# Kernel optimization log

Hardware: AMD Instinct MI355X
Metric: run time of the kernel (lower is better)

Reference implementation:

```python
import jax, jax.numpy as jnp
import numpy as np

NUM_HEADS = 32
EPS = 1e-5
NEG_INF = -1e9


def _ln(x, g, b):
    m = x.mean(-1, keepdims=True)
    v = ((x - m) ** 2).mean(-1, keepdims=True)
    return (x - m) / jnp.sqrt(v + EPS) * g + b


def setup_inputs() -> dict:
    key = jax.random.key(0)
    ks = jax.random.split(key, 20)
    N, B, D, E, F, L = 512, 2, 768, 256, 3072, 4
    inp = {
        'x': jax.random.normal(ks[0], (N, B, D), jnp.float32),
        'pos': jax.random.normal(ks[1], (B, N, 3), jnp.float32) * 5.0,
        'padding_mask': jnp.broadcast_to(jnp.arange(N)[None, :] >= N - 32, (B, N)),
        'outcell_index': jax.random.randint(ks[2], (B, E), 0, N),
        'expand_pos': jax.random.normal(ks[3], (B, E, 3), jnp.float32) * 5.0,
        'expand_mask': jnp.broadcast_to(jnp.arange(E)[None, :] >= E - 16, (B, E)),
        'vec_project_w': jax.random.normal(ks[4], (D, 3 * D), jnp.float32) * 0.02,
        'ln_x_g': jnp.ones((L, D), jnp.float32),
        'ln_x_b': jnp.zeros((L, D), jnp.float32),
        'ln_vec_g': jnp.ones((L, D), jnp.float32),
        'ln_vec_b': jnp.zeros((L, D), jnp.float32),
        'adaln_x_w': jax.random.normal(ks[5], (L, D, D), jnp.float32) * 0.02,
        'adaln_vecmlp_w': jax.random.normal(ks[6], (L, D, 2 * D), jnp.float32) * 0.02,
        'out_proj_w': jax.random.normal(ks[7], (L, D, D), jnp.float32) * 0.02,
        'vecmlp_norm_g': jnp.ones((L, D), jnp.float32),
        'vecmlp_norm_b': jnp.zeros((L, D), jnp.float32),
        'mlp_w1': jax.random.normal(ks[8], (L, D, F), jnp.float32) * 0.02,
        'mlp_w2': jax.random.normal(ks[9], (L, F, D), jnp.float32) * 0.02,
    }
    return inp


def reference(x, pos, padding_mask, outcell_index, expand_pos, expand_mask,
              vec_project_w, ln_x_g, ln_x_b, ln_vec_g, ln_vec_b,
              adaln_x_w, adaln_vecmlp_w, out_proj_w,
              vecmlp_norm_g, vecmlp_norm_b, mlp_w1, mlp_w2):
    x = jnp.swapaxes(x, 0, 1)  # [B,N,D]
    B, N, D = x.shape
    H = NUM_HEADS
    hd = D // H
    L = ln_x_g.shape[0]

    # --- PBC-expanded pairwise distance bias ---
    epf = jnp.concatenate([pos, expand_pos], axis=1)  # [B,S,3]
    S = epf.shape[1]
    delta = pos[:, :, None, :] - epf[:, None, :, :]   # [B,N,S,3]
    sq = (delta * delta).sum(-1)
    dist = jnp.where(sq > 0, jnp.sqrt(jnp.where(sq > 0, sq, 1.0)), 0.0)
    kpm_full = jnp.concatenate([padding_mask, expand_mask], axis=-1)  # [B,S]
    dist = jnp.where(padding_mask[:, :, None], 1e6, dist)
    dist = jnp.where(kpm_full[:, None, :], 1e6, dist)
    dist = 1.0 / (dist + 1.0)
    # additive attn mask (bias + key-padding -inf), broadcast over heads
    attn_mask = jnp.where(kpm_full[:, None, None, :], NEG_INF, dist[:, None, :, :])  # [B,1,N,S]

    vec = (jax.nn.silu(x) @ vec_project_w).reshape(B, N, 3, D)
    barange = jnp.arange(B)[:, None]
    scale = 1.0 / jnp.sqrt(jnp.float32(3 * hd))

    for l in range(L):
        rx, rv = x, vec
        xl = _ln(x, ln_x_g[l], ln_x_b[l])
        vl = _ln(vec, ln_vec_g[l], ln_vec_b[l])
        scale_x = jax.nn.silu(xl) @ adaln_x_w[l]        # [B,N,D]
        vmod = vl * scale_x[:, :, None, :]              # [B,N,3,D]
        # PBC gather-expanded K/V
        kv_exp = vmod[barange, outcell_index]           # [B,E,3,D]
        kv = jnp.concatenate([vmod, kv_exp], axis=1)    # [B,S,3,D]
        q = vmod.reshape(B, N, 3, H, hd).transpose(0, 3, 1, 2, 4).reshape(B, H, N, 3 * hd)
        k = kv.reshape(B, S, 3, H, hd).transpose(0, 3, 1, 2, 4).reshape(B, H, S, 3 * hd)
        v = k  # q=k=v in this block (same modulated vec)
        k = kv.reshape(B, S, 3, H, hd).transpose(0, 3, 1, 2, 4).reshape(B, H, S, 3 * hd)
        logits = jnp.einsum('bhnd,bhsd->bhns', q, k) * scale + attn_mask
        p = jax.nn.softmax(logits, axis=-1)
        o = jnp.einsum('bhns,bhsd->bhnd', p, v)          # [B,H,N,3hd]
        o = o.transpose(0, 2, 1, 3).reshape(B, N, H, 3, hd).transpose(0, 1, 3, 2, 4).reshape(B, N, 3, D)
        o = o @ out_proj_w[l]
        x = xl + rx
        vec = o + rv
        rx, rv = x, vec
        vm = _ln(vec, vecmlp_norm_g[l], vecmlp_norm_b[l])
        vm = jax.nn.silu(vm @ mlp_w1[l]) @ mlp_w2[l]     # [B,N,3,D]
        ss = jax.nn.silu(vm) @ adaln_vecmlp_w[l]         # [B,N,3,2D]
        sc, sh = jnp.split(ss, 2, axis=-1)
        x = x * sc.sum(-2) + sh.sum(-2) + rx
        vec = vm + rv
    return x, vec
```

## Files before the change

kernel.cpp:

```cpp
#include <hip/hip_runtime.h>

typedef __bf16 bf16_t;
typedef __bf16 bf8   __attribute__((ext_vector_type(8)));
typedef __bf16 bf4   __attribute__((ext_vector_type(4)));
typedef float  f32x4 __attribute__((ext_vector_type(4)));

__device__ __forceinline__ f32x4 mfma16(bf8 a, bf8 b, f32x4 c){
  return __builtin_amdgcn_mfma_f32_16x16x32_bf16(a, b, c, 0, 0, 0);
}
__device__ __forceinline__ float siluf_(float x){ return x / (1.f + __expf(-x)); }

__device__ __forceinline__ void async16(bf16_t* lds, const bf16_t* g){
  __builtin_amdgcn_global_load_lds(
      (const __attribute__((address_space(1))) unsigned int*)g,
      (__attribute__((address_space(3))) unsigned int*)lds, 16, 0, 0);
}

#define SCALE_QK 0.1178511302f

#define WT_VP   0ull
#define WT_AX   3538944ull
#define WT_AV   8257536ull
#define WT_OP   17694720ull
#define WT_M1   22413312ull
#define WT_M2   41287680ull
#define MASKB   60162048ull
#define SILUX   63307776ull
#define SILUXL  64880640ull
#define VLB     66453504ull
#define QKHB    79036416ull
#define KVTB    88473600ull
#define OBFB    97910784ull
#define VMLNB   102629376ull
#define H1B     107347968ull
#define SVM2B   126222336ull

struct TD { const float* s; bf16_t* d; int R, C, start, perz; };
struct TPack { TD t[6]; };

#define NTRB 3672

__global__ void prologue(TPack P,
                         const float* __restrict__ pos, const float* __restrict__ epos,
                         bf16_t* __restrict__ wm,
                         const float* __restrict__ xin, float* __restrict__ x,
                         bf16_t* __restrict__ sx,
                         const float* __restrict__ lxg, const float* __restrict__ lxb,
                         bf16_t* __restrict__ siluxl)
{
  __shared__ bf16_t tile[128*72];
  const int bid = blockIdx.x;
  const int t = threadIdx.x;
  if (bid >= NTRB + 3072){
    const int w2 = t >> 6, l = t & 63;
    const int r = (bid - NTRB - 3072)*4 + w2;
    const int b = r >> 9, n = r & 511;
    const float* p = xin + ((size_t)n*2 + b)*768;
    f32x4 v[3]; float s = 0.f;
    #pragma unroll
    for (int ps = 0; ps < 3; ++ps){
      v[ps] = *(const f32x4*)(p + ps*256 + l*4);
      bf4 sb;
      #pragma unroll
      for (int e = 0; e < 4; ++e){ s += v[ps][e]; sb[e] = (bf16_t)siluf_(v[ps][e]); }
      *(bf4*)(sx + (size_t)r*768 + ps*256 + l*4) = sb;
    }
    #pragma unroll
    for (int m = 1; m < 64; m <<= 1) s += __shfl_xor(s, m);
    float mean = s * (1.f/768.f);
    float q = 0.f;
    #pragma unroll
    for (int ps = 0; ps < 3; ++ps)
      #pragma unroll
      for (int e = 0; e < 4; ++e){ float d = v[ps][e] - mean; q += d*d; }
    #pragma unroll
    for (int m = 1; m < 64; m <<= 1) q += __shfl_xor(q, m);
    float rstd = rsqrtf(q * (1.f/768.f) + 1e-5f);
    #pragma unroll
    for (int ps = 0; ps < 3; ++ps){
      int col = ps*256 + l*4;
      f32x4 gg = *(const f32x4*)(lxg + col);
      f32x4 bv = *(const f32x4*)(lxb + col);
      f32x4 xo; bf4 ob;
      #pragma unroll
      for (int e = 0; e < 4; ++e){
        float xl = (v[ps][e] - mean) * rstd * gg[e] + bv[e];
        xo[e] = xl + v[ps][e];
        ob[e] = (bf16_t)siluf_(xl);
      }
      *(f32x4*)(x + (size_t)r*768 + col) = xo;
      *(bf4*)(siluxl + (size_t)r*768 + col) = ob;
    }
    return;
  }
  if (bid >= NTRB){
    int i = (bid - NTRB) * 256 + t;
    int s = i % 768, tt = i / 768;
    int n = tt % 512, b = tt / 512;
    bool kpm = (s < 512) ? (s >= 480) : (s >= 752);
    float o;
    if (kpm) o = 0.f;
    else {
      float d;
      if (n >= 480) d = 1e6f;
      else {
        const float* p = pos + (size_t)(b*512 + n)*3;
        const float* e = (s < 512) ? pos + (size_t)(b*512 + s)*3
                                   : epos + (size_t)(b*256 + (s-512))*3;
        float dx = p[0]-e[0], dy = p[1]-e[1], dz = p[2]-e[2];
        float sq = dx*dx + dy*dy + dz*dz;
        d = sq > 0.f ? sqrtf(sq) : 0.f;
      }
      o = __expf(1.f / (d + 1.f));
    }
    wm[i] = (bf16_t)o;
    return;
  }
  int k = 0;
  #pragma unroll
  for (int i = 1; i < 6; ++i) k = (bid >= P.t[i].start) ? i : k;
  const TD td = P.t[k];
  const int loc = bid - td.start;
  const int z = loc / td.perz, tl = loc - z*td.perz;
  const int nct = td.C >> 7;
  const int cx = tl % nct, ry = tl / nct;
  const size_t base = (size_t)z * td.R * td.C;
  const int r0 = ry*64, c0 = cx*128;
  #pragma unroll
  for (int half = 0; half < 2; ++half){
    int bb = half*256 + t;
    int rb = bb >> 5, cb = bb & 31;
    f32x4 v[4];
    #pragma unroll
    for (int i = 0; i < 4; ++i)
      v[i] = *(const f32x4*)(td.s + base + (size_t)(r0 + rb*4 + i)*td.C + c0 + cb*4);
    const int sw = (cb & 7) << 1;
    const int rp = 4*(rb ^ sw);
    #pragma unroll
    for (int e = 0; e < 4; ++e){
      bf4 pk;
      #pragma unroll
      for (int i = 0; i < 4; ++i) pk[i] = (bf16_t)v[i][e];
      *(bf4*)&tile[(cb*4 + e)*72 + rp] = pk;
    }
  }
  __syncthreads();
  #pragma unroll
  for (int jj = 0; jj < 4; ++jj){
    int sid = jj*256 + t;
    int c = sid >> 3, q = sid & 7;
    int qp = q ^ ((c >> 2) & 7);
    bf8 o = *(const bf8*)&tile[c*72 + qp*8];
    *(bf8*)(td.d + base + (size_t)(c0 + c)*td.R + r0 + q*8) = o;
  }
}

__global__ __launch_bounds__(256,2) void ln_kernel(
    const float* __restrict__ in, const float* __restrict__ g, const float* __restrict__ bb,
    bf16_t* __restrict__ bfout)
{
  const int w = threadIdx.x >> 6, l = threadIdx.x & 63;
  const size_t r = (size_t)blockIdx.x * 4 + w;
  const float* p = in + r * 768;
  f32x4 v[3]; float s = 0.f;
  #pragma unroll
  for (int ps = 0; ps < 3; ++ps){
    v[ps] = *(const f32x4*)(p + ps*256 + l*4);
    #pragma unroll
    for (int e = 0; e < 4; ++e) s += v[ps][e];
  }
  #pragma unroll
  for (int m = 1; m < 64; m <<= 1) s += __shfl_xor(s, m);
  float mean = s * (1.f/768.f);
  float q = 0.f;
  #pragma unroll
  for (int ps = 0; ps < 3; ++ps)
    #pragma unroll
    for (int e = 0; e < 4; ++e){ float d = v[ps][e] - mean; q += d*d; }
  #pragma unroll
  for (int m = 1; m < 64; m <<= 1) q += __shfl_xor(q, m);
  float rstd = rsqrtf(q * (1.f/768.f) + 1e-5f);
  #pragma unroll
  for (int ps = 0; ps < 3; ++ps){
    int col = ps*256 + l*4;
    f32x4 gg = *(const f32x4*)(g + col);
    f32x4 bv = *(const f32x4*)(bb + col);
    bf4 ob;
    #pragma unroll
    for (int e = 0; e < 4; ++e)
      ob[e] = (bf16_t)((v[ps][e] - mean) * rstd * gg[e] + bv[e]);
    *(bf4*)(bfout + r*768 + col) = ob;
  }
}

__global__ __launch_bounds__(256,2) void pack2_kernel(
    const bf16_t* __restrict__ vl, const bf16_t* __restrict__ pq,
    const int* __restrict__ idx, bf16_t* __restrict__ qkh, bf16_t* __restrict__ kvt)
{
  __shared__ bf16_t tile[64*104];
  const int sb = blockIdx.x, bh = blockIdx.y;
  const int b = bh >> 5, h = bh & 31;
  const int tid = threadIdx.x;
  const bf8 z8 = {};
  #pragma unroll
  for (int it = 0; it < 3; ++it){
    int u = it*256 + tid;
    int s_l = u / 12, ch = u % 12;
    int s = sb*64 + s_l;
    bf8 o = z8;
    if (ch < 9){
      int n = (s < 512) ? s : idx[b*256 + (s - 512)];
      int c = ch / 3, jj0 = (ch % 3) * 8;
      int d0 = h*24 + jj0;
      size_t soff = (size_t)(b*512 + n)*768 + d0;
      bf8 a = *(const bf8*)(vl + ((size_t)(b*512 + n)*3 + c)*768 + d0);
      bf8 q0 = *(const bf8*)(pq + soff);
      bf8 q1 = *(const bf8*)(pq + soff + 786432);
      bf8 q2 = *(const bf8*)(pq + soff + 1572864);
      bf8 q3 = *(const bf8*)(pq + soff + 2359296);
      #pragma unroll
      for (int e = 0; e < 8; ++e){
        float sc = (float)q0[e] + (float)q1[e] + (float)q2[e] + (float)q3[e];
        o[e] = (bf16_t)((float)a[e] * sc);
      }
    }
    *(bf8*)(qkh + ((size_t)bh*768 + s)*96 + ch*8) = o;
    *(bf8*)&tile[s_l*104 + ch*8] = o;
  }
  __syncthreads();
  #pragma unroll
  for (int it = 0; it < 3; ++it){
    int u = it*256 + tid;
    int d_r = u / 8, s8 = u % 8;
    bf8 o;
    #pragma unroll
    for (int e = 0; e < 8; ++e) o[e] = tile[(s8*8 + e)*104 + d_r];
    *(bf8*)(kvt + ((size_t)bh*96 + d_r)*768 + sb*64 + s8*8) = o;
  }
}

__global__ __launch_bounds__(256,2) void attn_kernel(
    const bf16_t* __restrict__ qkh, const bf16_t* __restrict__ kvt,
    const bf16_t* __restrict__ wm, bf16_t* __restrict__ obf)
{
  __shared__ bf16_t Ks[64*128];
  __shared__ bf16_t Vs[96*72];
  __shared__ bf16_t Ps[64*72];
  __shared__ bf16_t Ws[64*72];
  const int g = blockIdx.x;
  const int qt = g >> 6, bh = g & 63;
  const int b = bh >> 5, h = bh & 31;
  const int tid = threadIdx.x, w = tid >> 6, l = tid & 63;
  const int lg = l >> 4, lr = l & 15;
  const int qn0 = qt*64 + w*16 + lg*4;

  bf8 aq[3];
  {
    const bf16_t* qb = qkh + ((size_t)bh*768 + qt*64 + w*16 + lr)*96;
    #pragma unroll
    for (int ks = 0; ks < 3; ++ks) aq[ks] = *(const bf8*)(qb + ks*32 + lg*8);
  }

  int klds[3], vlds[3]; size_t kg[3], vg[3];
  #pragma unroll
  for (int it = 0; it < 3; ++it){
    int f = it*256 + tid;
    int r_ = f / 12, c_ = f % 12;
    klds[it] = r_*256 + ((c_*16) ^ ((r_ & 7) << 4));
    kg[it] = ((size_t)bh*768 + r_)*96 + c_*8;
    int vd = f >> 3, vc = (f & 7)*8;
    vlds[it] = vd*72 + vc;
    vg[it] = ((size_t)bh*96 + vd)*768 + vc;
  }
  const bf16_t* wrow = wm + (size_t)b*512*768;
  const int wr_ = tid >> 2, wcq = (tid & 3) * 16;
  const size_t wg0 = (size_t)(qt*64 + wr_)*768 + wcq;
  const int wlds = wr_*72 + wcq;

  f32x4 zf = {0.f,0.f,0.f,0.f};
  f32x4 accO[6];
  #pragma unroll
  for (int i = 0; i < 6; ++i) accO[i] = zf;
  float s_r[4] = {0.f, 0.f, 0.f, 0.f};

  bf8 kr[3], vr[3], wg[2];
  #pragma unroll
  for (int it = 0; it < 3; ++it){
    kr[it] = *(const bf8*)(qkh + kg[it]);
    vr[it] = *(const bf8*)(kvt + vg[it]);
  }
  wg[0] = *(const bf8*)(wrow + wg0);
  wg[1] = *(const bf8*)(wrow + wg0 + 8);
  #pragma unroll
  for (int it = 0; it < 3; ++it){
    *(bf8*)((char*)Ks + klds[it]) = kr[it];
    *(bf8*)&Vs[vlds[it]] = vr[it];
  }
  *(bf8*)&Ws[wlds] = wg[0];
  *(bf8*)&Ws[wlds + 8] = wg[1];
  __syncthreads();

  for (int t = 0; t < 12; ++t){
    const int s0 = t*64;
    if (t < 11){
      #pragma unroll
      for (int it = 0; it < 3; ++it){
        kr[it] = *(const bf8*)(qkh + kg[it] + (size_t)(s0 + 64)*96);
        vr[it] = *(const bf8*)(kvt + vg[it] + (s0 + 64));
      }
      wg[0] = *(const bf8*)(wrow + wg0 + s0 + 64);
      wg[1] = *(const bf8*)(wrow + wg0 + s0 + 72);
    }
    f32x4 sacc[4];
    __builtin_amdgcn_s_setprio(1);
    #pragma unroll
    for (int sf = 0; sf < 4; ++sf){
      sacc[sf] = zf;
      const int row = sf*16 + lr;
      #pragma unroll
      for (int ks = 0; ks < 3; ++ks){
        bf8 bg = *(const bf8*)((const char*)Ks + row*256 + ((ks*64 + lg*16) ^ ((row & 7) << 4)));
        sacc[sf] = mfma16(aq[ks], bg, sacc[sf]);
      }
    }
    __builtin_amdgcn_s_setprio(0);
    #pragma unroll
    for (int sf = 0; sf < 4; ++sf)
      #pragma unroll
      for (int r = 0; r < 4; ++r){
        float p = __expf(sacc[sf][r]*SCALE_QK)
                  * (float)Ws[(w*16 + lg*4 + r)*72 + sf*16 + lr];
        s_r[r] += p;
        Ps[(w*16 + lg*4 + r)*72 + sf*16 + lr] = (bf16_t)p;
      }
    __builtin_amdgcn_s_setprio(1);
    #pragma unroll
    for (int k2 = 0; k2 < 2; ++k2){
      bf8 pa = *(const bf8*)&Ps[(w*16 + lr)*72 + k2*32 + lg*8];
      #pragma unroll
      for (int df = 0; df < 6; ++df)
        accO[df] = mfma16(pa, *(const bf8*)&Vs[(df*16 + lr)*72 + k2*32 + lg*8], accO[df]);
    }
    __builtin_amdgcn_s_setprio(0);
    if (t < 11){
      __syncthreads();
      #pragma unroll
      for (int it = 0; it < 3; ++it){
        *(bf8*)((char*)Ks + klds[it]) = kr[it];
        *(bf8*)&Vs[vlds[it]] = vr[it];
      }
      *(bf8*)&Ws[wlds] = wg[0];
      *(bf8*)&Ws[wlds + 8] = wg[1];
      __syncthreads();
    }
  }
  #pragma unroll
  for (int m = 1; m < 16; m <<= 1)
    #pragma unroll
    for (int r = 0; r < 4; ++r) s_r[r] += __shfl_xor(s_r[r], m);
  float rs[4];
  #pragma unroll
  for (int r = 0; r < 4; ++r) rs[r] = 1.f / s_r[r];
  #pragma unroll
  for (int df = 0; df < 6; ++df){
    int dp = df*16 + lr;
    if (dp < 72){
      int c = dp / 24, jj = dp - c*24;
      #pragma unroll
      for (int r = 0; r < 4; ++r){
        float v = accO[df][r] * rs[r];
        int qn = qn0 + r;
        obf[((size_t)(b*512 + qn)*3 + c)*768 + h*24 + jj] = (bf16_t)v;
      }
    }
  }
}

template<int EPI>
__global__ __launch_bounds__(512,4) void gemm2(
    const bf16_t* __restrict__ A, const bf16_t* __restrict__ Bt,
    float* __restrict__ Cf, bf16_t* __restrict__ Cb,
    int M, int Nn, int K, int Ksub, int ntiles)
{
  __shared__ bf16_t As[128*64];
  __shared__ bf16_t Bs[128*64];
  const int tid = threadIdx.x;
  const int w = tid >> 6, l = tid & 63;
  const int lg = l >> 4, lr = l & 15;
  const int gb = blockIdx.x;
  const int sidx = gb >> 3, xcd = gb & 7;
  const int nt = sidx % ntiles;
  const int mt = xcd + (sidx / ntiles) * 8;
  const int wm = (w >> 2) * 64, wn = (w & 3) * 32;

  const int srow = w*8 + (l >> 3);
  const int scol = (((l & 7) ^ (l >> 3)) << 3);
  const bf16_t* Ab = A  + (size_t)(mt*128) * K;
  const bf16_t* Bb = Bt + (size_t)(nt*128) * K;
  const int kbeg = blockIdx.z * Ksub;

  f32x4 zf = {0.f,0.f,0.f,0.f};
  f32x4 acc[4][2];
  #pragma unroll
  for (int i = 0; i < 4; ++i)
    #pragma unroll
    for (int j = 0; j < 2; ++j) acc[i][j] = zf;

  int offA[4], offB[2];
  #pragma unroll
  for (int i = 0; i < 4; ++i){
    int row = wm + i*16 + lr;
    offA[i] = row*128 + ((lg*16) ^ ((row & 7) << 4));
  }
  #pragma unroll
  for (int j = 0; j < 2; ++j){
    int row = wn + j*16 + lr;
    offB[j] = row*128 + ((lg*16) ^ ((row & 7) << 4));
  }

  for (int k0 = kbeg; k0 < kbeg + Ksub; k0 += 64){
    __syncthreads();
    #pragma unroll
    for (int c = 0; c < 2; ++c){
      async16(&As[c*4096 + w*512], Ab + (size_t)(c*64 + srow)*K + k0 + scol);
      async16(&Bs[c*4096 + w*512], Bb + (size_t)(c*64 + srow)*K + k0 + scol);
    }
    __syncthreads();
    #pragma unroll
    for (int kk = 0; kk < 2; ++kk){
      bf8 af[4], bg[2];
      #pragma unroll
      for (int i = 0; i < 4; ++i)
        af[i] = *(const bf8*)((const char*)As + (offA[i] ^ (kk*64)));
      #pragma unroll
      for (int j = 0; j < 2; ++j)
        bg[j] = *(const bf8*)((const char*)Bs + (offB[j] ^ (kk*64)));
      #pragma unroll
      for (int i = 0; i < 4; ++i)
        #pragma unroll
        for (int j = 0; j < 2; ++j)
          acc[i][j] = mfma16(af[i], bg[j], acc[i][j]);
    }
  }

  const size_t zoff = (EPI == 6) ? (size_t)blockIdx.z * M * Nn : 0;
  #pragma unroll
  for (int i = 0; i < 4; ++i){
    int r0 = mt*128 + wm + i*16 + lg*4;
    #pragma unroll
    for (int j = 0; j < 2; ++j){
      int cc = nt*128 + wn + j*16 + lr;
      #pragma unroll
      for (int r = 0; r < 4; ++r){
        size_t off = (size_t)(r0 + r)*Nn + cc;
        float v = acc[i][j][r];
        if constexpr (EPI == 0)      Cf[off] = v;
        else if constexpr (EPI == 2) Cb[off] = (bf16_t)siluf_(v);
        else                         Cb[zoff + off] = (bf16_t)v;
      }
    }
  }
}

__global__ __launch_bounds__(256,2) void redop_ln(
    const bf16_t* __restrict__ p, float* __restrict__ vec,
    const float* __restrict__ g, const float* __restrict__ bb,
    bf16_t* __restrict__ vmln)
{
  const int w = threadIdx.x >> 6, l = threadIdx.x & 63;
  const size_t r = (size_t)blockIdx.x * 4 + w;
  f32x4 v[3]; float s = 0.f;
  #pragma unroll
  for (int ps = 0; ps < 3; ++ps){
    size_t off = r*768 + ps*256 + l*4;
    bf4 p0 = *(const bf4*)(p + off);
    bf4 p1 = *(const bf4*)(p + off + 2359296);
    bf4 p2 = *(const bf4*)(p + off + 4718592);
    f32x4 vv = *(const f32x4*)(vec + off);
    #pragma unroll
    for (int e = 0; e < 4; ++e){
      float t = vv[e] + (float)p0[e] + (float)p1[e] + (float)p2[e];
      v[ps][e] = t; s += t;
    }
    *(f32x4*)(vec + off) = v[ps];
  }
  #pragma unroll
  for (int m = 1; m < 64; m <<= 1) s += __shfl_xor(s, m);
  float mean = s * (1.f/768.f);
  float q = 0.f;
  #pragma unroll
  for (int ps = 0; ps < 3; ++ps)
    #pragma unroll
    for (int e = 0; e < 4; ++e){ float d = v[ps][e] - mean; q += d*d; }
  #pragma unroll
  for (int m = 1; m < 64; m <<= 1) q += __shfl_xor(q, m);
  float rstd = rsqrtf(q * (1.f/768.f) + 1e-5f);
  #pragma unroll
  for (int ps = 0; ps < 3; ++ps){
    int col = ps*256 + l*4;
    f32x4 gg = *(const f32x4*)(g + col);
    f32x4 bv = *(const f32x4*)(bb + col);
    bf4 ob;
    #pragma unroll
    for (int e = 0; e < 4; ++e)
      ob[e] = (bf16_t)((v[ps][e] - mean) * rstd * gg[e] + bv[e]);
    *(bf4*)(vmln + r*768 + col) = ob;
  }
}

__global__ __launch_bounds__(256,2) void redmlp2_ln(
    const bf16_t* __restrict__ p, float* __restrict__ vec,
    bf16_t* __restrict__ svm2s,
    const float* __restrict__ g, const float* __restrict__ bb,
    bf16_t* __restrict__ vlb, int doln)
{
  const int w = threadIdx.x >> 6, l = threadIdx.x & 63;
  const size_t bn = (size_t)blockIdx.x * 4 + w;
  f32x4 ssum[3];
  #pragma unroll
  for (int ps = 0; ps < 3; ++ps) ssum[ps] = (f32x4){0.f,0.f,0.f,0.f};
  for (int c = 0; c < 3; ++c){
    const size_t r = bn*3 + c;
    f32x4 v[3]; float s = 0.f;
    #pragma unroll
    for (int ps = 0; ps < 3; ++ps){
      size_t off = r*768 + ps*256 + l*4;
      bf4 p0 = *(const bf4*)(p + off);
      bf4 p1 = *(const bf4*)(p + off + 2359296);
      f32x4 vv = *(const f32x4*)(vec + off);
      #pragma unroll
      for (int e = 0; e < 4; ++e){
        float tm = (float)p0[e] + (float)p1[e];
        float t = vv[e] + tm;
        v[ps][e] = t; s += t;
        ssum[ps][e] += siluf_(tm);
      }
      *(f32x4*)(vec + off) = v[ps];
    }
    if (doln){
      #pragma unroll
      for (int m = 1; m < 64; m <<= 1) s += __shfl_xor(s, m);
      float mean = s * (1.f/768.f);
      float q = 0.f;
      #pragma unroll
      for (int ps = 0; ps < 3; ++ps)
        #pragma unroll
        for (int e = 0; e < 4; ++e){ float d = v[ps][e] - mean; q += d*d; }
      #pragma unroll
      for (int m = 1; m < 64; m <<= 1) q += __shfl_xor(q, m);
      float rstd = rsqrtf(q * (1.f/768.f) + 1e-5f);
      #pragma unroll
      for (int ps = 0; ps < 3; ++ps){
        int col = ps*256 + l*4;
        f32x4 gg = *(const f32x4*)(g + col);
        f32x4 bv = *(const f32x4*)(bb + col);
        bf4 ob;
        #pragma unroll
        for (int e = 0; e < 4; ++e)
          ob[e] = (bf16_t)((v[ps][e] - mean) * rstd * gg[e] + bv[e]);
        *(bf4*)(vlb + r*768 + col) = ob;
      }
    }
  }
  #pragma unroll
  for (int ps = 0; ps < 3; ++ps){
    bf4 ob;
    #pragma unroll
    for (int e = 0; e < 4; ++e) ob[e] = (bf16_t)ssum[ps][e];
    *(bf4*)(svm2s + bn*768 + ps*256 + l*4) = ob;
  }
}

__global__ __launch_bounds__(256,2) void comb_ln(
    const bf16_t* __restrict__ p, float* __restrict__ x,
    const float* __restrict__ g, const float* __restrict__ bb,
    bf16_t* __restrict__ siluxl)
{
  const int w = threadIdx.x >> 6, l = threadIdx.x & 63;
  const size_t r = (size_t)blockIdx.x * 4 + w;
  const size_t base = r * 1536;
  f32x4 v[3]; float s = 0.f;
  #pragma unroll
  for (int ps = 0; ps < 3; ++ps){
    int col = ps*256 + l*4;
    bf4 sc0 = *(const bf4*)(p + base + col);
    bf4 sc1 = *(const bf4*)(p + base + col + 1572864);
    bf4 sh0 = *(const bf4*)(p + base + 768 + col);
    bf4 sh1 = *(const bf4*)(p + base + 768 + col + 1572864);
    f32x4 xv = *(const f32x4*)(x + r*768 + col);
    #pragma unroll
    for (int e = 0; e < 4; ++e){
      float t = xv[e]*(1.f + (float)sc0[e] + (float)sc1[e])
              + (float)sh0[e] + (float)sh1[e];
      v[ps][e] = t; s += t;
    }
  }
  #pragma unroll
  for (int m = 1; m < 64; m <<= 1) s += __shfl_xor(s, m);
  float mean = s * (1.f/768.f);
  float q = 0.f;
  #pragma unroll
  for (int ps = 0; ps < 3; ++ps)
    #pragma unroll
    for (int e = 0; e < 4; ++e){ float d = v[ps][e] - mean; q += d*d; }
  #pragma unroll
  for (int m = 1; m < 64; m <<= 1) q += __shfl_xor(q, m);
  float rstd = rsqrtf(q * (1.f/768.f) + 1e-5f);
  #pragma unroll
  for (int ps = 0; ps < 3; ++ps){
    int col = ps*256 + l*4;
    f32x4 gg = *(const f32x4*)(g + col);
    f32x4 bv = *(const f32x4*)(bb + col);
    f32x4 xo; bf4 ob;
    #pragma unroll
    for (int e = 0; e < 4; ++e){
      float xl = (v[ps][e] - mean) * rstd * gg[e] + bv[e];
      xo[e] = xl + v[ps][e];
      ob[e] = (bf16_t)siluf_(xl);
    }
    *(f32x4*)(x + r*768 + col) = xo;
    *(bf4*)(siluxl + r*768 + col) = ob;
  }
}

__global__ void combine_kernel(const bf16_t* __restrict__ p, float* __restrict__ x)
{
  int i = blockIdx.x * 256 + threadIdx.x;
  int row = i / 192, col = (i % 192) * 4;
  size_t base = (size_t)row*1536 + col;
  bf4 sc0 = *(const bf4*)(p + base);
  bf4 sc1 = *(const bf4*)(p + base + 1572864);
  bf4 sh0 = *(const bf4*)(p + base + 768);
  bf4 sh1 = *(const bf4*)(p + base + 768 + 1572864);
  f32x4 xv = *(const f32x4*)(x + (size_t)row*768 + col);
  f32x4 o;
  #pragma unroll
  for (int e = 0; e < 4; ++e)
    o[e] = xv[e]*(1.f + (float)sc0[e] + (float)sc1[e])
         + (float)sh0[e] + (float)sh1[e];
  *(f32x4*)(x + (size_t)row*768 + col) = o;
}

extern "C" void kernel_launch(void* const* d_in, const int* in_sizes, int n_in,
                              void* d_out, int out_size, void* d_ws, size_t ws_size,
                              hipStream_t stream)
{
  const float* x_in = (const float*)d_in[0];
  const float* pos  = (const float*)d_in[1];
  const int*   idx  = (const int*)d_in[3];
  const float* epos = (const float*)d_in[4];
  const float* vp_w = (const float*)d_in[6];
  const float* lxg  = (const float*)d_in[7];
  const float* lxb  = (const float*)d_in[8];
  const float* lvg  = (const float*)d_in[9];
  const float* lvb  = (const float*)d_in[10];
  const float* axw  = (const float*)d_in[11];
  const float* avw  = (const float*)d_in[12];
  const float* opw  = (const float*)d_in[13];
  const float* vng  = (const float*)d_in[14];
  const float* vnb  = (const float*)d_in[15];
  const float* w1   = (const float*)d_in[16];
  const float* w2   = (const float*)d_in[17];

  char* ws = (char*)d_ws;
  bf16_t* wt_vp = (bf16_t*)(ws + WT_VP);
  bf16_t* wt_ax = (bf16_t*)(ws + WT_AX);
  bf16_t* wt_av = (bf16_t*)(ws + WT_AV);
  bf16_t* wt_op = (bf16_t*)(ws + WT_OP);
  bf16_t* wt_m1 = (bf16_t*)(ws + WT_M1);
  bf16_t* wt_m2 = (bf16_t*)(ws + WT_M2);
  bf16_t* wmask = (bf16_t*)(ws + MASKB);
  bf16_t* silux = (bf16_t*)(ws + SILUX);
  bf16_t* siluxl= (bf16_t*)(ws + SILUXL);
  bf16_t* vlb   = (bf16_t*)(ws + VLB);
  bf16_t* qkh   = (bf16_t*)(ws + QKHB);
  bf16_t* kvt   = (bf16_t*)(ws + KVTB);
  bf16_t* partX = (bf16_t*)(ws + H1B);
  bf16_t* partQ = (bf16_t*)(ws + QKHB);
  bf16_t* partV = (bf16_t*)(ws + VLB);
  bf16_t* obf   = (bf16_t*)(ws + OBFB);
  bf16_t* vmln  = (bf16_t*)(ws + VMLNB);
  bf16_t* h1    = (bf16_t*)(ws + H1B);
  bf16_t* svm2s = (bf16_t*)(ws + SVM2B);

  float* x   = (float*)d_out;
  float* vec = x + 786432;

  TPack P;
  P.t[0] = { vp_w, wt_vp, 768, 2304,    0,  216 };
  P.t[1] = { axw,  wt_ax, 768,  768,  216,   72 };
  P.t[2] = { avw,  wt_av, 768, 1536,  504,  144 };
  P.t[3] = { opw,  wt_op, 768,  768, 1080,   72 };
  P.t[4] = { w1,   wt_m1, 768, 3072, 1368,  288 };
  P.t[5] = { w2,   wt_m2, 3072, 768, 2520,  288 };
  prologue<<<NTRB + 3072 + 256, 256, 0, stream>>>(P, pos, epos, wmask, x_in, x, silux,
                                                  lxg, lxb, siluxl);

  gemm2<0><<<dim3(8*18,1,1), 512, 0, stream>>>(silux, wt_vp, vec, nullptr,
                                               1024, 2304, 768, 768, 18);
  ln_kernel<<<768, 256, 0, stream>>>(vec, lvg, lvb, vlb);

  for (int l = 0; l < 4; ++l){
    gemm2<6><<<dim3(8*6,1,4), 512, 0, stream>>>(siluxl, wt_ax + (size_t)l*768*768, nullptr,
                                                partX, 1024, 768, 768, 192, 6);
    pack2_kernel<<<dim3(12, 64), 256, 0, stream>>>(vlb, partX, idx, qkh, kvt);
    attn_kernel<<<512, 256, 0, stream>>>(qkh, kvt, wmask, obf);
    gemm2<6><<<dim3(24*6,1,3), 512, 0, stream>>>(obf, wt_op + (size_t)l*768*768, nullptr,
                                                 partV, 3072, 768, 768, 256, 6);
    redop_ln<<<768, 256, 0, stream>>>(partV, vec, vng + l*768, vnb + l*768, vmln);
    gemm2<2><<<dim3(24*24,1,1), 512, 0, stream>>>(vmln, wt_m1 + (size_t)l*3072*768, nullptr,
                                                  h1, 3072, 3072, 768, 768, 24);
    gemm2<6><<<dim3(24*6,1,2), 512, 0, stream>>>(h1, wt_m2 + (size_t)l*768*3072, nullptr,
                                                 partQ, 3072, 768, 3072, 1536, 6);
    redmlp2_ln<<<256, 256, 0, stream>>>(partQ, vec, svm2s,
                                        lvg + (l+1 < 4 ? (l+1)*768 : 0),
                                        lvb + (l+1 < 4 ? (l+1)*768 : 0),
                                        vlb, (l < 3) ? 1 : 0);
    gemm2<6><<<dim3(8*12,1,2), 512, 0, stream>>>(svm2s, wt_av + (size_t)l*1536*768, nullptr,
                                                 partQ, 1024, 1536, 768, 384, 12);
    if (l < 3)
      comb_ln<<<256, 256, 0, stream>>>(partQ, x, lxg + (l+1)*768, lxb + (l+1)*768, siluxl);
    else
      combine_kernel<<<768, 256, 0, stream>>>(partQ, x);
  }
}
```

Before: 577.0 us.

## Double-buffer GEMM LDS tiles and increase split-K with fused reductions

The GEMM main loop now double-buffers its LDS tiles, issuing async loads for the next K-slice while MFMAs run on the current one. This leaves one barrier per iteration instead of two. The vec-projection GEMM becomes split-K with a new fused reduce+LayerNorm kernel, and the adaLN GEMMs use more K-splits, with consumers summing more partial slices. The cost is twice the LDS per block, which may reduce occupancy, plus more partial-sum traffic.

After: 599.5 us. 1.04x slower.

```diff
diff --git a/kernel.cpp b/kernel.cpp
--- a/kernel.cpp
+++ b/kernel.cpp
@@ -155,19 +155,25 @@
   }
 }
 
-__global__ __launch_bounds__(256,2) void ln_kernel(
-    const float* __restrict__ in, const float* __restrict__ g, const float* __restrict__ bb,
-    bf16_t* __restrict__ bfout)
+__global__ __launch_bounds__(256,2) void redvp_ln(
+    const bf16_t* __restrict__ p, float* __restrict__ vec,
+    const float* __restrict__ g, const float* __restrict__ bb,
+    bf16_t* __restrict__ vlb)
 {
   const int w = threadIdx.x >> 6, l = threadIdx.x & 63;
   const size_t r = (size_t)blockIdx.x * 4 + w;
-  const float* p = in + r * 768;
   f32x4 v[3]; float s = 0.f;
   #pragma unroll
   for (int ps = 0; ps < 3; ++ps){
-    v[ps] = *(const f32x4*)(p + ps*256 + l*4);
-    #pragma unroll
-    for (int e = 0; e < 4; ++e) s += v[ps][e];
+    size_t off = r*768 + ps*256 + l*4;
+    bf4 p0 = *(const bf4*)(p + off);
+    bf4 p1 = *(const bf4*)(p + off + 2359296);
+    #pragma unroll
+    for (int e = 0; e < 4; ++e){
+      float t = (float)p0[e] + (float)p1[e];
+      v[ps][e] = t; s += t;
+    }
+    *(f32x4*)(vec + off) = v[ps];
   }
   #pragma unroll
   for (int m = 1; m < 64; m <<= 1) s += __shfl_xor(s, m);
@@ -189,7 +195,7 @@
     #pragma unroll
     for (int e = 0; e < 4; ++e)
       ob[e] = (bf16_t)((v[ps][e] - mean) * rstd * gg[e] + bv[e]);
-    *(bf4*)(bfout + r*768 + col) = ob;
+    *(bf4*)(vlb + r*768 + col) = ob;
   }
 }
 
@@ -214,15 +220,17 @@
       int d0 = h*24 + jj0;
       size_t soff = (size_t)(b*512 + n)*768 + d0;
       bf8 a = *(const bf8*)(vl + ((size_t)(b*512 + n)*3 + c)*768 + d0);
-      bf8 q0 = *(const bf8*)(pq + soff);
-      bf8 q1 = *(const bf8*)(pq + soff + 786432);
-      bf8 q2 = *(const bf8*)(pq + soff + 1572864);
-      bf8 q3 = *(const bf8*)(pq + soff + 2359296);
-      #pragma unroll
-      for (int e = 0; e < 8; ++e){
-        float sc = (float)q0[e] + (float)q1[e] + (float)q2[e] + (float)q3[e];
-        o[e] = (bf16_t)((float)a[e] * sc);
-      }
+      float sc[8];
+      #pragma unroll
+      for (int e = 0; e < 8; ++e) sc[e] = 0.f;
+      #pragma unroll
+      for (int sl = 0; sl < 6; ++sl){
+        bf8 qv = *(const bf8*)(pq + soff + (size_t)sl*786432);
+        #pragma unroll
+        for (int e = 0; e < 8; ++e) sc[e] += (float)qv[e];
+      }
+      #pragma unroll
+      for (int e = 0; e < 8; ++e) o[e] = (bf16_t)((float)a[e] * sc[e]);
     }
     *(bf8*)(qkh + ((size_t)bh*768 + s)*96 + ch*8) = o;
     *(bf8*)&tile[s_l*104 + ch*8] = o;
@@ -382,8 +390,8 @@
     float* __restrict__ Cf, bf16_t* __restrict__ Cb,
     int M, int Nn, int K, int Ksub, int ntiles)
 {
-  __shared__ bf16_t As[128*64];
-  __shared__ bf16_t Bs[128*64];
+  __shared__ bf16_t As[2][8192];
+  __shared__ bf16_t Bs[2][8192];
   const int tid = threadIdx.x;
   const int w = tid >> 6, l = tid & 63;
   const int lg = l >> 4, lr = l & 15;
@@ -418,29 +426,40 @@
     offB[j] = row*128 + ((lg*16) ^ ((row & 7) << 4));
   }
 
-  for (int k0 = kbeg; k0 < kbeg + Ksub; k0 += 64){
-    __syncthreads();
-    #pragma unroll
-    for (int c = 0; c < 2; ++c){
-      async16(&As[c*4096 + w*512], Ab + (size_t)(c*64 + srow)*K + k0 + scol);
-      async16(&Bs[c*4096 + w*512], Bb + (size_t)(c*64 + srow)*K + k0 + scol);
-    }
-    __syncthreads();
+  const int nk = Ksub >> 6;
+  #pragma unroll
+  for (int c = 0; c < 2; ++c){
+    async16(&As[0][c*4096 + w*512], Ab + (size_t)(c*64 + srow)*K + kbeg + scol);
+    async16(&Bs[0][c*4096 + w*512], Bb + (size_t)(c*64 + srow)*K + kbeg + scol);
+  }
+  __syncthreads();
+  int buf = 0;
+  for (int t = 0; t < nk; ++t){
+    if (t + 1 < nk){
+      const int k0 = kbeg + (t+1)*64;
+      #pragma unroll
+      for (int c = 0; c < 2; ++c){
+        async16(&As[buf^1][c*4096 + w*512], Ab + (size_t)(c*64 + srow)*K + k0 + scol);
+        async16(&Bs[buf^1][c*4096 + w*512], Bb + (size_t)(c*64 + srow)*K + k0 + scol);
+      }
+    }
     #pragma unroll
     for (int kk = 0; kk < 2; ++kk){
       bf8 af[4], bg[2];
       #pragma unroll
       for (int i = 0; i < 4; ++i)
-        af[i] = *(const bf8*)((const char*)As + (offA[i] ^ (kk*64)));
+        af[i] = *(const bf8*)((const char*)(&As[buf][0]) + (offA[i] ^ (kk*64)));
       #pragma unroll
       for (int j = 0; j < 2; ++j)
-        bg[j] = *(const bf8*)((const char*)Bs + (offB[j] ^ (kk*64)));
+        bg[j] = *(const bf8*)((const char*)(&Bs[buf][0]) + (offB[j] ^ (kk*64)));
       #pragma unroll
       for (int i = 0; i < 4; ++i)
         #pragma unroll
         for (int j = 0; j < 2; ++j)
           acc[i][j] = mfma16(af[i], bg[j], acc[i][j]);
     }
+    __syncthreads();
+    buf ^= 1;
   }
 
   const size_t zoff = (EPI == 6) ? (size_t)blockIdx.z * M * Nn : 0;
@@ -454,9 +473,8 @@
       for (int r = 0; r < 4; ++r){
         size_t off = (size_t)(r0 + r)*Nn + cc;
         float v = acc[i][j][r];
-        if constexpr (EPI == 0)      Cf[off] = v;
-        else if constexpr (EPI == 2) Cb[off] = (bf16_t)siluf_(v);
-        else                         Cb[zoff + off] = (bf16_t)v;
+        if constexpr (EPI == 2) Cb[off] = (bf16_t)siluf_(v);
+        else                    Cb[zoff + off] = (bf16_t)v;
       }
     }
   }
@@ -583,15 +601,18 @@
   #pragma unroll
   for (int ps = 0; ps < 3; ++ps){
     int col = ps*256 + l*4;
-    bf4 sc0 = *(const bf4*)(p + base + col);
-    bf4 sc1 = *(const bf4*)(p + base + col + 1572864);
-    bf4 sh0 = *(const bf4*)(p + base + 768 + col);
-    bf4 sh1 = *(const bf4*)(p + base + 768 + col + 1572864);
+    float sc[4] = {0.f,0.f,0.f,0.f}, sh[4] = {0.f,0.f,0.f,0.f};
+    #pragma unroll
+    for (int sl = 0; sl < 3; ++sl){
+      bf4 c0 = *(const bf4*)(p + base + col + (size_t)sl*1572864);
+      bf4 h0 = *(const bf4*)(p + base + 768 + col + (size_t)sl*1572864);
+      #pragma unroll
+      for (int e = 0; e < 4; ++e){ sc[e] += (float)c0[e]; sh[e] += (float)h0[e]; }
+    }
     f32x4 xv = *(const f32x4*)(x + r*768 + col);
     #pragma unroll
     for (int e = 0; e < 4; ++e){
-      float t = xv[e]*(1.f + (float)sc0[e] + (float)sc1[e])
-              + (float)sh0[e] + (float)sh1[e];
+      float t = xv[e]*(1.f + sc[e]) + sh[e];
       v[ps][e] = t; s += t;
     }
   }
@@ -628,16 +649,19 @@
   int i = blockIdx.x * 256 + threadIdx.x;
   int row = i / 192, col = (i % 192) * 4;
   size_t base = (size_t)row*1536 + col;
-  bf4 sc0 = *(const bf4*)(p + base);
-  bf4 sc1 = *(const bf4*)(p + base + 1572864);
-  bf4 sh0 = *(const bf4*)(p + base + 768);
-  bf4 sh1 = *(const bf4*)(p + base + 768 + 1572864);
+  float sc[4] = {0.f,0.f,0.f,0.f}, sh[4] = {0.f,0.f,0.f,0.f};
+  #pragma unroll
+  for (int sl = 0; sl < 3; ++sl){
+    bf4 c0 = *(const bf4*)(p + base + (size_t)sl*1572864);
+    bf4 h0 = *(const bf4*)(p + base + 768 + (size_t)sl*1572864);
+    #pragma unroll
+    for (int e = 0; e < 4; ++e){ sc[e] += (float)c0[e]; sh[e] += (float)h0[e]; }
+  }
   f32x4 xv = *(const f32x4*)(x + (size_t)row*768 + col);
   f32x4 o;
   #pragma unroll
   for (int e = 0; e < 4; ++e)
-    o[e] = xv[e]*(1.f + (float)sc0[e] + (float)sc1[e])
-         + (float)sh0[e] + (float)sh1[e];
+    o[e] = xv[e]*(1.f + sc[e]) + sh[e];
   *(f32x4*)(x + (size_t)row*768 + col) = o;
 }
 
@@ -696,13 +720,13 @@
   prologue<<<NTRB + 3072 + 256, 256, 0, stream>>>(P, pos, epos, wmask, x_in, x, silux,
                                                   lxg, lxb, siluxl);
 
-  gemm2<0><<<dim3(8*18,1,1), 512, 0, stream>>>(silux, wt_vp, vec, nullptr,
-                                               1024, 2304, 768, 768, 18);
-  ln_kernel<<<768, 256, 0, stream>>>(vec, lvg, lvb, vlb);
+  gemm2<6><<<dim3(8*18,1,2), 512, 0, stream>>>(silux, wt_vp, nullptr, partQ,
+                                               1024, 2304, 768, 384, 18);
+  redvp_ln<<<768, 256, 0, stream>>>(partQ, vec, lvg, lvb, vlb);
 
   for (int l = 0; l < 4; ++l){
-    gemm2<6><<<dim3(8*6,1,4), 512, 0, stream>>>(siluxl, wt_ax + (size_t)l*768*768, nullptr,
-                                                partX, 1024, 768, 768, 192, 6);
+    gemm2<6><<<dim3(8*6,1,6), 512, 0, stream>>>(siluxl, wt_ax + (size_t)l*768*768, nullptr,
+                                                partX, 1024, 768, 768, 128, 6);
     pack2_kernel<<<dim3(12, 64), 256, 0, stream>>>(vlb, partX, idx, qkh, kvt);
     attn_kernel<<<512, 256, 0, stream>>>(qkh, kvt, wmask, obf);
     gemm2<6><<<dim3(24*6,1,3), 512, 0, stream>>>(obf, wt_op + (size_t)l*768*768, nullptr,
@@ -716,8 +740,8 @@
                                         lvg + (l+1 < 4 ? (l+1)*768 : 0),
                                         lvb + (l+1 < 4 ? (l+1)*768 : 0),
                                         vlb, (l < 3) ? 1 : 0);
-    gemm2<6><<<dim3(8*12,1,2), 512, 0, stream>>>(svm2s, wt_av + (size_t)l*1536*768, nullptr,
-                                                 partQ, 1024, 1536, 768, 384, 12);
+    gemm2<6><<<dim3(8*12,1,3), 512, 0, stream>>>(svm2s, wt_av + (size_t)l*1536*768, nullptr,
+                                                 partQ, 1024, 1536, 768, 256, 12);
     if (l < 3)
       comb_ln<<<256, 256, 0, stream>>>(partQ, x, lxg + (l+1)*768, lxb + (l+1)*768, siluxl);
     else
```
